# Optimization experiments

Hardware: AMD Instinct MI355X
Metric: run time of the kernel (lower is better)

## Reference

```python
import jax, jax.numpy as jnp
import numpy as np

# Dimensions: B=batch, T=timesteps, D=input_dim, U=units, R=recurrent_size, NE=#edge types
B, T, D, U, R, NE = 1024, 128, 256, 256, 4, 40


def setup_inputs() -> dict:
    key = jax.random.key(0)
    ks = jax.random.split(key, 11)
    s = 1.0 / np.sqrt(U)  # RandomUniform(-1/sqrt(units), 1/sqrt(units)) as in __init__
    inputs = jax.random.normal(ks[0], (B, T, D), jnp.float32)
    input_lengths = jax.random.randint(ks[1], (B,), 1, T + 1)
    # dependencies[b, t, k] indexes a PAST timestep (< t) whose hidden state feeds step t;
    # values >= t are treated as '$' (no dependency -> zero state), matching the string-'$' logic.
    dependencies = jax.random.randint(ks[2], (B, T, R - 1), 0, T)
    edge_types = jax.random.randint(ks[3], (B, T, R), 0, NE)
    mask = jax.random.randint(ks[4], (B, T), 0, 2).astype(bool)
    cell_mask = jax.random.randint(ks[5], (B, T, R), 0, 2).astype(bool)
    Wx = jax.random.uniform(ks[6], (D, 3 * U), jnp.float32, -s, s)   # input kernel (r,z,h)
    Uh = jax.random.uniform(ks[7], (U, 3 * U), jnp.float32, -s, s)   # recurrent kernel (r,z,h)
    Ve = jax.random.uniform(ks[8], (U, 3 * U), jnp.float32, -s, s)   # edge-embedding kernel (r,z,h)
    b = jax.random.uniform(ks[9], (3 * U,), jnp.float32, -s, s)
    edge_emb = jax.random.normal(ks[10], (NE, U), jnp.float32) * 0.02  # shared_emb table
    return dict(inputs=inputs, input_lengths=input_lengths, dependencies=dependencies,
                edge_types=edge_types, mask=mask, cell_mask=cell_mask,
                Wx=Wx, Uh=Uh, Ve=Ve, b=b, edge_emb=edge_emb)


def _graph_gru_forward(inputs, dependencies, edge_types, mask, cell_mask, Wx, Uh, Ve, b, edge_emb):
    Bn, Tn, Dn = inputs.shape
    Un = Uh.shape[0]
    # time-major, as the wrapper does with swap_batch_timestep
    xg_t = jnp.einsum('btd,dg->tbg', inputs, Wx) + b   # precompute input projections [T,B,3U]
    dep_t = jnp.swapaxes(dependencies, 0, 1)           # [T,B,R-1]
    et_t = jnp.swapaxes(edge_types, 0, 1)              # [T,B,R]
    m_t = jnp.swapaxes(mask, 0, 1)                     # [T,B]
    cm_t = jnp.swapaxes(cell_mask, 0, 1)               # [T,B,R]
    bidx = jnp.arange(Bn)

    def step(carry, xs):
        h_prev, H = carry                  # h_prev: [B,U]; H: running history of states [T,B,U]
        t, xg, dep, et, m, cm = xs
        # gather dependency states from history; dep >= t means '$' -> zero state
        valid = dep < t                                        # [B,R-1]
        dep_states = H[jnp.clip(dep, 0, Tn - 1), bidx[:, None]]  # [B,R-1,U]
        dep_states = jnp.where(valid[..., None], dep_states, 0.0)
        hs = jnp.concatenate([h_prev[:, None, :], dep_states], axis=1)  # states tuple -> [B,R,U]
        cmf = cm.astype(hs.dtype)[..., None]                   # per-slot cell mask [B,R,1]
        hs_m = hs * cmf
        e_m = edge_emb[et] * cmf                               # [B,R,U]
        # aggregate messages from the R masked (state, edge-embedding) slots into the 3 gates
        msg = jnp.einsum('bru,ug->bg', hs_m, Uh) + jnp.einsum('bru,ug->bg', e_m, Ve)  # [B,3U]
        xr, xz, xh = jnp.split(xg, 3, axis=-1)
        mr, mz, mh = jnp.split(msg, 3, axis=-1)
        r = jax.nn.sigmoid(xr + mr)
        z = jax.nn.sigmoid(xz + mz)
        hcand = jnp.tanh(xh + r * mh)
        denom = jnp.maximum(cmf.sum(axis=1), 1.0)              # [B,1]
        h_bar = hs_m.sum(axis=1) / denom                       # mean of active predecessor states
        h_new = z * h_bar + (1.0 - z) * hcand
        # masked update: where(mask_t, new_state, previous return state)
        h_out = jnp.where(m[:, None], h_new, h_prev)
        H = H.at[t].set(h_out)
        return (h_out, H), None

    h0 = jnp.zeros((Bn, Un), inputs.dtype)
    H0 = jnp.zeros((Tn, Bn, Un), inputs.dtype)
    (h_last, _), _ = jax.lax.scan(
        step, (h0, H0), (jnp.arange(Tn), xg_t, dep_t, et_t, m_t, cm_t))
    # zero_output_for_mask on the last output (return_sequences=False)
    return jnp.where(m_t[-1][:, None], h_last, 0.0)


def reference(inputs, input_lengths, dependencies, edge_types, mask, cell_mask,
              Wx, Uh, Ve, b, edge_emb):
    # input_lengths only matters when go_backwards=True (default False) -> unused.
    del input_lengths
    return _graph_gru_forward(inputs, dependencies, edge_types, mask, cell_mask,
                              Wx, Uh, Ve, b, edge_emb)
```

## Files before the change

kernel.cpp:

```cpp
#include <hip/hip_runtime.h>
#include <hip/hip_bf16.h>
#include <stdint.h>

typedef _Float16 f16;
typedef _Float16 f16x8 __attribute__((ext_vector_type(8)));
typedef _Float16 f16x4 __attribute__((ext_vector_type(4)));
typedef float    f32x4 __attribute__((ext_vector_type(4)));

#define B_N 1024
#define T_N 128
#define U_N 256
#define G3  768
#define NC  1024
#define KC  512
#define M_N (B_N * T_N)
#define S16P 264

__device__ __forceinline__ void glds16(const void* g, void* l) {
  __builtin_amdgcn_global_load_lds((const __attribute__((address_space(1))) unsigned int*)g,
                                   (__attribute__((address_space(3))) unsigned int*)l, 16, 0, 0);
}
__device__ __forceinline__ void glds4(const void* g, void* l) {
  __builtin_amdgcn_global_load_lds((const __attribute__((address_space(1))) unsigned int*)g,
                                   (__attribute__((address_space(3))) unsigned int*)l, 4, 0, 0);
}

__global__ void k_prep(const float* __restrict__ Wx, const float* __restrict__ Uh,
                       const float* __restrict__ Ve, const float* __restrict__ bsrc,
                       f16* __restrict__ B2, float* __restrict__ bias, f16* __restrict__ UhF)
{
  int idx = blockIdx.x * 256 + threadIdx.x;
  if (idx < NC * KC) {
    int e = idx & 7, slot = (idx >> 3) & 3, r = (idx >> 5) & 127;
    int kt = (idx >> 12) & 15, nt8 = idx >> 16;
    int swz = ((r >> 2) ^ r) & 3;
    int np = nt8 * 128 + r;
    int k  = kt * 32 + ((slot ^ swz) & 3) * 8 + e;
    int u = np >> 2, part = np & 3;
    float v;
    if (part == 0)      v = (k < 256) ? Wx[k * G3 + u]         : Ve[(k - 256) * G3 + u];
    else if (part == 1) v = (k < 256) ? Wx[k * G3 + 256 + u]   : Ve[(k - 256) * G3 + 256 + u];
    else if (part == 2) v = (k < 256) ? Wx[k * G3 + 512 + u]   : 0.f;
    else                v = (k < 256) ? 0.f                    : Ve[(k - 256) * G3 + 512 + u];
    B2[idx] = (f16)v;
    return;
  }
  int i2 = idx - NC * KC;
  if (i2 < U_N * G3) {
    int j = i2 & 7, lane = (i2 >> 3) & 63, fn = i2 >> 9;
    int nt = fn % 6, kkw = fn / 6;
    int kk = kkw & 7, w = kkw >> 3;
    int k = kk * 32 + (lane >> 4) * 8 + j;
    int npp = w * 96 + nt * 16 + (lane & 15);
    int q = npp >> 4;
    int u = (q / 3) * 16 + (npp & 15), gate = q % 3;
    UhF[i2] = (f16)Uh[k * G3 + gate * 256 + u];
    return;
  }
  int i3 = i2 - U_N * G3;
  if (i3 < NC) {
    int u = i3 >> 2, part = i3 & 3;
    bias[i3] = (part < 3) ? bsrc[part * 256 + u] : 0.f;
  }
}

__global__ __launch_bounds__(256) void k_build_a2(const float* __restrict__ inp, const int* __restrict__ et,
                           const int* __restrict__ cmk, const float* __restrict__ emb,
                           f16* __restrict__ A2)
{
  int idx = blockIdx.x * 256 + threadIdx.x;
  int slot = idx & 3, t = (idx >> 2) & 127, kt = (idx >> 9) & 15, b = idx >> 13;
  int swz = ((t >> 2) ^ t) & 3;
  int k0 = kt * 32 + ((slot ^ swz) & 3) * 8;
  int m = b * 128 + t;
  f16x8 v;
  if (k0 < 256) {
    const float* s = inp + (size_t)m * 256 + k0;
    #pragma unroll
    for (int j = 0; j < 8; ++j) v[j] = (f16)s[j];
  } else {
    int c = k0 - 256;
    const int* e  = et  + (size_t)m * 4;
    const int* cm = cmk + (size_t)m * 4;
    float a[8] = {0,0,0,0,0,0,0,0};
    #pragma unroll
    for (int r = 0; r < 4; ++r)
      if (cm[r]) {
        const float* es = emb + e[r] * U_N + c;
        #pragma unroll
        for (int j = 0; j < 8; ++j) a[j] += es[j];
      }
    #pragma unroll
    for (int j = 0; j < 8; ++j) v[j] = (f16)a[j];
  }
  *(f16x8*)(A2 + (size_t)idx * 8) = v;
}

__global__ __launch_bounds__(256) void k_gemm2(const f16* __restrict__ A2,
                                               const f16* __restrict__ B2,
                                               const float* __restrict__ bias,
                                               f16* __restrict__ C)
{
  __shared__ __align__(16) f16 sbuf[3][2][4096];
  const int tid  = threadIdx.x;
  const int lane = tid & 63, wv = tid >> 6;
  const int wm = wv >> 1, wn = wv & 1;
  const int l15 = lane & 15, lhi = lane >> 4;
  const int wg = (blockIdx.x & 7) * 1024 + (blockIdx.x >> 3);
  const int mt = wg >> 3, nt = wg & 7;
  const int m0 = mt * 128, n0 = nt * 128;

  const f16* gabase = A2 + (size_t)mt * 16 * 4096 + wv * 1024 + lane * 8;
  const f16* gbbase = B2 + (size_t)nt * 16 * 4096 + wv * 1024 + lane * 8;

  #define STAGE(kt_, buf_) do {                                             \
    int kk_ = (kt_);                                                        \
    glds16(gabase + (size_t)kk_ * 4096,       &sbuf[buf_][0][wv * 1024]);   \
    glds16(gabase + (size_t)kk_ * 4096 + 512, &sbuf[buf_][0][wv * 1024 + 512]); \
    glds16(gbbase + (size_t)kk_ * 4096,       &sbuf[buf_][1][wv * 1024]);   \
    glds16(gbbase + (size_t)kk_ * 4096 + 512, &sbuf[buf_][1][wv * 1024 + 512]); \
  } while (0)

  f32x4 acc[4][4] = {};

  STAGE(0, 0);
  STAGE(1, 1);
  __builtin_amdgcn_sched_barrier(0);

  int aoff[4], boff[4];
  #pragma unroll
  for (int i = 0; i < 4; ++i) {
    int ar = wm * 64 + i * 16 + l15;
    aoff[i] = ar * 32 + ((lhi ^ ((ar >> 2) ^ ar)) & 3) * 8;
    int br = wn * 64 + i * 16 + l15;
    boff[i] = br * 32 + ((lhi ^ ((br >> 2) ^ br)) & 3) * 8;
  }

  for (int t = 0; t < 16; ++t) {
    const int buf  = t % 3;
    const int bufp = (t + 2) % 3;
    STAGE((t + 2 < 16) ? (t + 2) : 15, bufp);
    __builtin_amdgcn_sched_barrier(0);
    asm volatile("s_waitcnt vmcnt(8)" ::: "memory");
    __builtin_amdgcn_sched_barrier(0);
    __builtin_amdgcn_s_barrier();
    __builtin_amdgcn_sched_barrier(0);

    const f16* sA = &sbuf[buf][0][0];
    const f16* sB = &sbuf[buf][1][0];
    f16x8 af[4], bf[4];
    #pragma unroll
    for (int i = 0; i < 4; ++i) {
      af[i] = *(const f16x8*)(sA + aoff[i]);
      bf[i] = *(const f16x8*)(sB + boff[i]);
    }
    #pragma unroll
    for (int i = 0; i < 4; ++i)
      #pragma unroll
      for (int j = 0; j < 4; ++j)
        acc[i][j] = __builtin_amdgcn_mfma_f32_16x16x32_f16(af[i], bf[j], acc[i][j], 0, 0, 0);

    asm volatile("s_waitcnt lgkmcnt(0)" ::: "memory");
    __builtin_amdgcn_s_barrier();
    __builtin_amdgcn_sched_barrier(0);
  }

  float bv[4];
  #pragma unroll
  for (int j = 0; j < 4; ++j) bv[j] = bias[n0 + wn * 64 + j * 16 + l15];
  asm volatile("s_waitcnt vmcnt(0)" ::: "memory");
  __builtin_amdgcn_sched_barrier(0);
  __builtin_amdgcn_s_barrier();

  f16* ep = &sbuf[0][0][0];
  #pragma unroll
  for (int i = 0; i < 4; ++i)
    #pragma unroll
    for (int j = 0; j < 4; ++j)
      #pragma unroll
      for (int r = 0; r < 4; ++r)
        ep[(wm * 64 + i * 16 + lhi * 4 + r) * 132 + wn * 64 + j * 16 + l15] =
            (f16)(acc[i][j][r] + bv[j]);
  __syncthreads();

  #pragma unroll
  for (int it = 0; it < 8; ++it) {
    int row = it * 16 + (tid >> 4), chunk = tid & 15;
    *(f16x8*)(C + (size_t)(m0 + row) * 1024 + n0 + chunk * 8) =
        *(const f16x8*)(ep + row * 132 + chunk * 8);
  }
  #undef STAGE
}

__global__ __launch_bounds__(512, 2) void k_scan4(
    const f16* __restrict__ pre,
    const f16* __restrict__ UhF,
    const int* __restrict__ dep,
    const int* __restrict__ cmk,
    const int* __restrict__ msk,
    f16* __restrict__ H16,
    float* __restrict__ out)
{
  __shared__ __align__(16) f16 s16[16 * S16P];
  __shared__ __align__(16) f16 hring[2][1024];
  __shared__ __align__(16) f16 dbuf[2][3072];
  __shared__ __align__(16) f16 spre[3][4096];
  __shared__ __align__(16) int sidxl[4][64];
  __shared__ __align__(16) int dpad[64];

  const int tid  = threadIdx.x;
  const int lane = tid & 63, w = tid >> 6;
  const int l15  = lane & 15, lhi = lane >> 4;
  const int b0   = blockIdx.x * 4;

  f16x8 uh[48];
  {
    const f16* ub = UhF + ((size_t)w * 48 * 64 + lane) * 8;
    #pragma unroll
    for (int i = 0; i < 48; ++i) uh[i] = *(const f16x8*)(ub + i * 512);
  }

  ((int*)hring)[tid]       = 0;
  ((int*)hring)[tid + 512] = 0;

  if (tid < 96) {
    int tt = tid >> 5, ll2 = tid & 31, rr = ll2 >> 3, f = ll2 & 7;
    size_t b = b0 + rr;
    int v;
    if (f < 4)      v = cmk[(b * T_N + tt) * 4 + f];
    else if (f < 7) v = dep[(b * T_N + tt) * 3 + (f - 4)];
    else            v = msk[b * T_N + tt];
    sidxl[tt][rr * 8 + f] = v;
  }
  __syncthreads();

  const f16* spre_src = pre + ((size_t)(b0 + (w >> 1)) * T_N) * 1024 + (w & 1) * 512 + lane * 8;
  const int  ll = lane & 31;
  const int  srr = ll >> 3, sf = ll & 7;
  const size_t sb = b0 + srr;
  const int* sidx_base;
  int sidx_stride;
  if (sf < 4)      { sidx_base = cmk + sb * T_N * 4 + sf;       sidx_stride = 4; }
  else if (sf < 7) { sidx_base = dep + sb * T_N * 3 + (sf - 4); sidx_stride = 3; }
  else             { sidx_base = msk + sb * T_N;                sidx_stride = 1; }
  const int dq  = 2 * w + (lane >> 5);
  const int drr = dq / 3, drm = dq - drr * 3;
  const f16* dsrc_base = H16 + (size_t)(b0 + drr) * 256 + (lane & 31) * 8;
  const int strr = ((w - 6) * 64 + lane) >> 5;
  const int stuo = (((w - 6) * 64 + lane) & 31) * 8;

  #pragma unroll
  for (int pr = 0; pr < 2; ++pr)
    glds16(spre_src + (size_t)pr * 1024, &spre[pr][w * 512]);
  #pragma unroll
  for (int i = 0; i < 3; ++i)
    glds4(msk, &dpad[0]);

  for (int t = 0; t < T_N; ++t) {
    asm volatile("s_waitcnt vmcnt(2)" ::: "memory");
    __builtin_amdgcn_sched_barrier(0);

    if (tid < 128) {
      const int rr = tid >> 5, uo = (tid & 31) * 8;
      const int* six = &sidxl[t & 3][rr * 8];
      int cm0 = six[0];
      int cms0 = six[1], cms1 = six[2], cms2 = six[3];
      int dd0 = six[4],  dd1 = six[5],  dd2 = six[6];
      f16x8 hprev = *(const f16x8*)&hring[(t + 1) & 1][rr * 256 + uo];
      f16x8 hold  = *(const f16x8*)&hring[t & 1][rr * 256 + uo];
      f32x4 a0 = {0.f,0.f,0.f,0.f}, a1 = {0.f,0.f,0.f,0.f};
      if (cm0) {
        #pragma unroll
        for (int j = 0; j < 4; ++j) { a0[j] += (float)hprev[j]; a1[j] += (float)hprev[j + 4]; }
      }
      int cma[3] = {cms0, cms1, cms2};
      int dda[3] = {dd0, dd1, dd2};
      #pragma unroll
      for (int r = 0; r < 3; ++r) {
        f16x8 dv = *(const f16x8*)&dbuf[t & 1][(rr * 3 + r) * 256 + uo];
        int d = dda[r];
        f16x8 src = (d == t - 1) ? hprev : ((d == t - 2) ? hold : dv);
        if (cma[r] && (d < t)) {
          #pragma unroll
          for (int j = 0; j < 4; ++j) { a0[j] += (float)src[j]; a1[j] += (float)src[j + 4]; }
        }
      }
      f16x8 s8;
      #pragma unroll
      for (int j = 0; j < 4; ++j) { s8[j] = (f16)a0[j]; s8[j + 4] = (f16)a1[j]; }
      *(f16x8*)&s16[(rr * 4) * S16P + uo] = s8;
    }
    asm volatile("s_waitcnt lgkmcnt(0)" ::: "memory");
    __builtin_amdgcn_s_barrier();
    __builtin_amdgcn_sched_barrier(0);

    if (w < 6) {
      int d = sidxl[(t + 1) & 3][drr * 8 + 4 + drm];
      glds16(dsrc_base + (size_t)d * (B_N * 256), &dbuf[(t + 1) & 1][w * 512]);
    } else {
      f16x8 hv = *(const f16x8*)&hring[(t + 1) & 1][strr * 256 + stuo];
      int tt = (t == 0) ? T_N : (t - 1);
      *(f16x8*)(H16 + ((size_t)tt * B_N + b0 + strr) * 256 + stuo) = hv;
    }
    __builtin_amdgcn_sched_barrier(0);
    {
      int tt2 = (t + 2 < T_N) ? (t + 2) : (T_N - 1);
      glds16(spre_src + (size_t)tt2 * 1024, &spre[(t + 2) % 3][w * 512]);
    }
    __builtin_amdgcn_sched_barrier(0);
    {
      int t3 = (t + 3 < T_N) ? (t + 3) : (T_N - 1);
      glds4(sidx_base + (size_t)t3 * sidx_stride, &sidxl[(t + 3) & 3][0]);
    }
    __builtin_amdgcn_sched_barrier(0);

    f32x4 acc[6];
    #pragma unroll
    for (int i = 0; i < 6; ++i) acc[i] = (f32x4){0.f, 0.f, 0.f, 0.f};
    #pragma unroll
    for (int kk = 0; kk < 8; ++kk) {
      f16x8 a = *(const f16x8*)(s16 + l15 * S16P + kk * 32 + lhi * 8);
      #pragma unroll
      for (int nt = 0; nt < 6; ++nt)
        acc[nt] = __builtin_amdgcn_mfma_f32_16x16x32_f16(a, uh[kk * 6 + nt], acc[nt], 0, 0, 0);
    }

    asm volatile("s_waitcnt vmcnt(7)" ::: "memory");
    __builtin_amdgcn_sched_barrier(0);
    {
      const int* six = &sidxl[t & 3][lhi * 8];
      int c0 = six[0], c1 = six[1], c2 = six[2], c3 = six[3];
      int mfl = six[7];
      float cnt  = (float)(c0 + c1 + c2 + c3);
      float rcnt = __builtin_amdgcn_rcpf(fmaxf(cnt, 1.f));
      #pragma unroll
      for (int ub2 = 0; ub2 < 2; ++ub2) {
        int u = w * 32 + ub2 * 16 + l15;
        f16x4 p = *(const f16x4*)&spre[t % 3][lhi * 1024 + u * 4];
        float mr = acc[ub2 * 3 + 0][0];
        float mz = acc[ub2 * 3 + 1][0];
        float mh = acc[ub2 * 3 + 2][0];
        float tr = (float)p.x + mr;
        float tz = (float)p.y + mz;
        float hx = (float)p.z;
        float he = (float)p.w;
        float rg = __builtin_amdgcn_rcpf(1.f + __expf(-tr));
        float zg = __builtin_amdgcn_rcpf(1.f + __expf(-tz));
        float aa = hx + rg * (mh + he);
        float hc = 2.f * __builtin_amdgcn_rcpf(1.f + __expf(-2.f * aa)) - 1.f;
        float sv = (float)s16[(lhi * 4) * S16P + u];
        float hb = sv * rcnt;
        float hn = zg * hb + (1.f - zg) * hc;
        float hp_ = (float)hring[(t + 1) & 1][lhi * 256 + u];
        float ho = mfl ? hn : hp_;
        hring[t & 1][lhi * 256 + u] = (f16)ho;
      }
    }
    asm volatile("s_waitcnt lgkmcnt(0)" ::: "memory");
    __builtin_amdgcn_s_barrier();
    __builtin_amdgcn_sched_barrier(0);
  }

  if (tid < 128) {
    const int rr = tid >> 5, uo = (tid & 31) * 8;
    int m = sidxl[(T_N - 1) & 3][rr * 8 + 7];
    f16x8 h8 = *(const f16x8*)&hring[(T_N - 1) & 1][rr * 256 + uo];
    f32x4 o0, o1;
    #pragma unroll
    for (int j = 0; j < 4; ++j) {
      o0[j] = m ? (float)h8[j]     : 0.f;
      o1[j] = m ? (float)h8[j + 4] : 0.f;
    }
    *(f32x4*)(out + (size_t)(b0 + rr) * 256 + uo)     = o0;
    *(f32x4*)(out + (size_t)(b0 + rr) * 256 + uo + 4) = o1;
  }
}

extern "C" void kernel_launch(void* const* d_in, const int* in_sizes, int n_in,
                              void* d_out, int out_size, void* d_ws, size_t ws_size,
                              hipStream_t stream)
{
  const float* inputs = (const float*)d_in[0];
  const int*   deps   = (const int*)d_in[2];
  const int*   et     = (const int*)d_in[3];
  const int*   msk    = (const int*)d_in[4];
  const int*   cmk    = (const int*)d_in[5];
  const float* Wx     = (const float*)d_in[6];
  const float* Uh     = (const float*)d_in[7];
  const float* Ve     = (const float*)d_in[8];
  const float* bb     = (const float*)d_in[9];
  const float* emb    = (const float*)d_in[10];
  float* out = (float*)d_out;

  char* ws = (char*)d_ws;
  f16*   A2    = (f16*)ws;
  f16*   H16   = (f16*)ws;
  f16*   pre   = (f16*)(ws + 134217728);
  f16*   B2    = (f16*)(ws + 402653184);
  float* bias  = (float*)(ws + 403701760);
  f16*   UhF   = (f16*)(ws + 403705856);

  int prep_n = NC * KC + U_N * G3 + NC;
  k_prep<<<dim3((prep_n + 255) / 256), dim3(256), 0, stream>>>(Wx, Uh, Ve, bb, B2, bias, UhF);
  k_build_a2<<<dim3(M_N * 64 / 256), dim3(256), 0, stream>>>(inputs, et, cmk, emb, A2);
  k_gemm2<<<dim3((M_N / 128) * (NC / 128)), dim3(256), 0, stream>>>(A2, B2, bias, pre);
  k_scan4<<<dim3(B_N / 4), dim3(512), 0, stream>>>(pre, UhF, deps, cmk, msk, H16, out);
}
```

Measured before the change: 507.3 us.

## Restructure scan kernel to four waves holding doubled recurrent weights in registers

```diff
diff --git a/kernel.cpp b/kernel.cpp
--- a/kernel.cpp
+++ b/kernel.cpp
@@ -19,10 +19,6 @@
 __device__ __forceinline__ void glds16(const void* g, void* l) {
   __builtin_amdgcn_global_load_lds((const __attribute__((address_space(1))) unsigned int*)g,
                                    (__attribute__((address_space(3))) unsigned int*)l, 16, 0, 0);
-}
-__device__ __forceinline__ void glds4(const void* g, void* l) {
-  __builtin_amdgcn_global_load_lds((const __attribute__((address_space(1))) unsigned int*)g,
-                                   (__attribute__((address_space(3))) unsigned int*)l, 4, 0, 0);
 }
 
 __global__ void k_prep(const float* __restrict__ Wx, const float* __restrict__ Uh,
@@ -48,10 +44,10 @@
   int i2 = idx - NC * KC;
   if (i2 < U_N * G3) {
     int j = i2 & 7, lane = (i2 >> 3) & 63, fn = i2 >> 9;
-    int nt = fn % 6, kkw = fn / 6;
+    int nt = fn % 12, kkw = fn / 12;
     int kk = kkw & 7, w = kkw >> 3;
     int k = kk * 32 + (lane >> 4) * 8 + j;
-    int npp = w * 96 + nt * 16 + (lane & 15);
+    int npp = w * 192 + nt * 16 + (lane & 15);
     int q = npp >> 4;
     int u = (q / 3) * 16 + (npp & 15), gate = q % 3;
     UhF[i2] = (f16)Uh[k * G3 + gate * 256 + u];
@@ -154,11 +150,13 @@
       af[i] = *(const f16x8*)(sA + aoff[i]);
       bf[i] = *(const f16x8*)(sB + boff[i]);
     }
+    __builtin_amdgcn_s_setprio(1);
     #pragma unroll
     for (int i = 0; i < 4; ++i)
       #pragma unroll
       for (int j = 0; j < 4; ++j)
         acc[i][j] = __builtin_amdgcn_mfma_f32_16x16x32_f16(af[i], bf[j], acc[i][j], 0, 0, 0);
+    __builtin_amdgcn_s_setprio(0);
 
     asm volatile("s_waitcnt lgkmcnt(0)" ::: "memory");
     __builtin_amdgcn_s_barrier();
@@ -192,7 +190,7 @@
   #undef STAGE
 }
 
-__global__ __launch_bounds__(512, 2) void k_scan4(
+__global__ __launch_bounds__(256, 1) void k_scan7(
     const f16* __restrict__ pre,
     const f16* __restrict__ UhF,
     const int* __restrict__ dep,
@@ -205,56 +203,50 @@
   __shared__ __align__(16) f16 hring[2][1024];
   __shared__ __align__(16) f16 dbuf[2][3072];
   __shared__ __align__(16) f16 spre[3][4096];
-  __shared__ __align__(16) int sidxl[4][64];
-  __shared__ __align__(16) int dpad[64];
+  __shared__ int sidx_all[4][T_N][8];
 
   const int tid  = threadIdx.x;
   const int lane = tid & 63, w = tid >> 6;
   const int l15  = lane & 15, lhi = lane >> 4;
   const int b0   = blockIdx.x * 4;
 
-  f16x8 uh[48];
+  f16x8 uh[96];
   {
-    const f16* ub = UhF + ((size_t)w * 48 * 64 + lane) * 8;
-    #pragma unroll
-    for (int i = 0; i < 48; ++i) uh[i] = *(const f16x8*)(ub + i * 512);
-  }
-
-  ((int*)hring)[tid]       = 0;
-  ((int*)hring)[tid + 512] = 0;
-
-  if (tid < 96) {
-    int tt = tid >> 5, ll2 = tid & 31, rr = ll2 >> 3, f = ll2 & 7;
+    const f16* ub = UhF + (size_t)w * 49152 + lane * 8;
+    #pragma unroll
+    for (int i = 0; i < 96; ++i) uh[i] = *(const f16x8*)(ub + i * 512);
+  }
+
+  for (int i = tid; i < 1024; i += 256) ((int*)hring)[i] = 0;
+  for (int i = tid; i < 2112; i += 256) ((int*)s16)[i] = 0;
+
+  for (int i = tid; i < 4 * T_N * 8; i += 256) {
+    int rr = i >> 10, rem = i & 1023, tt = rem >> 3, f = rem & 7;
     size_t b = b0 + rr;
     int v;
     if (f < 4)      v = cmk[(b * T_N + tt) * 4 + f];
     else if (f < 7) v = dep[(b * T_N + tt) * 3 + (f - 4)];
     else            v = msk[b * T_N + tt];
-    sidxl[tt][rr * 8 + f] = v;
+    sidx_all[rr][tt][f] = v;
   }
   __syncthreads();
-
-  const f16* spre_src = pre + ((size_t)(b0 + (w >> 1)) * T_N) * 1024 + (w & 1) * 512 + lane * 8;
-  const int  ll = lane & 31;
-  const int  srr = ll >> 3, sf = ll & 7;
-  const size_t sb = b0 + srr;
-  const int* sidx_base;
-  int sidx_stride;
-  if (sf < 4)      { sidx_base = cmk + sb * T_N * 4 + sf;       sidx_stride = 4; }
-  else if (sf < 7) { sidx_base = dep + sb * T_N * 3 + (sf - 4); sidx_stride = 3; }
-  else             { sidx_base = msk + sb * T_N;                sidx_stride = 1; }
-  const int dq  = 2 * w + (lane >> 5);
-  const int drr = dq / 3, drm = dq - drr * 3;
-  const f16* dsrc_base = H16 + (size_t)(b0 + drr) * 256 + (lane & 31) * 8;
-  const int strr = ((w - 6) * 64 + lane) >> 5;
-  const int stuo = (((w - 6) * 64 + lane) & 31) * 8;
-
-  #pragma unroll
-  for (int pr = 0; pr < 2; ++pr)
-    glds16(spre_src + (size_t)pr * 1024, &spre[pr][w * 512]);
-  #pragma unroll
-  for (int i = 0; i < 3; ++i)
-    glds4(msk, &dpad[0]);
+  __builtin_amdgcn_sched_barrier(0);
+
+  const f16* spre_src = pre + ((size_t)(b0 + w) * T_N) * 1024 + lane * 8;
+  const int  sprd = w * 1024;
+  const int q0 = 4 * w + (lane >> 5), q1 = q0 + 2;
+  const int r0 = q0 / 3, dm0 = q0 - r0 * 3;
+  const int r1 = q1 / 3, dm1 = q1 - r1 * 3;
+  const f16* dsrc0 = H16 + (size_t)(b0 + (r0 & 3)) * 256 + (lane & 31) * 8;
+  const f16* dsrc1 = H16 + (size_t)(b0 + (r1 & 3)) * 256 + (lane & 31) * 8;
+  const int srow0 = (lane >> 5), srow1 = 2 + (lane >> 5);
+  const int soff  = (lane & 31) * 8;
+
+  glds16(spre_src,        &spre[0][sprd]);
+  glds16(spre_src + 512,  &spre[0][sprd + 512]);
+  glds16(spre_src + 1024, &spre[1][sprd]);
+  glds16(spre_src + 1536, &spre[1][sprd + 512]);
+  __builtin_amdgcn_sched_barrier(0);
 
   for (int t = 0; t < T_N; ++t) {
     asm volatile("s_waitcnt vmcnt(2)" ::: "memory");
@@ -262,10 +254,10 @@
 
     if (tid < 128) {
       const int rr = tid >> 5, uo = (tid & 31) * 8;
-      const int* six = &sidxl[t & 3][rr * 8];
+      const int* six = &sidx_all[rr][t][0];
       int cm0 = six[0];
-      int cms0 = six[1], cms1 = six[2], cms2 = six[3];
-      int dd0 = six[4],  dd1 = six[5],  dd2 = six[6];
+      int cma[3] = {six[1], six[2], six[3]};
+      int dda[3] = {six[4], six[5], six[6]};
       f16x8 hprev = *(const f16x8*)&hring[(t + 1) & 1][rr * 256 + uo];
       f16x8 hold  = *(const f16x8*)&hring[t & 1][rr * 256 + uo];
       f32x4 a0 = {0.f,0.f,0.f,0.f}, a1 = {0.f,0.f,0.f,0.f};
@@ -273,8 +265,6 @@
         #pragma unroll
         for (int j = 0; j < 4; ++j) { a0[j] += (float)hprev[j]; a1[j] += (float)hprev[j + 4]; }
       }
-      int cma[3] = {cms0, cms1, cms2};
-      int dda[3] = {dd0, dd1, dd2};
       #pragma unroll
       for (int r = 0; r < 3; ++r) {
         f16x8 dv = *(const f16x8*)&dbuf[t & 1][(rr * 3 + r) * 256 + uo];
@@ -294,52 +284,53 @@
     __builtin_amdgcn_s_barrier();
     __builtin_amdgcn_sched_barrier(0);
 
-    if (w < 6) {
-      int d = sidxl[(t + 1) & 3][drr * 8 + 4 + drm];
-      glds16(dsrc_base + (size_t)d * (B_N * 256), &dbuf[(t + 1) & 1][w * 512]);
+    if (w < 3) {
+      int tn = (t + 1 < T_N) ? (t + 1) : (T_N - 1);
+      int d0v = sidx_all[r0][tn][4 + dm0];
+      glds16(dsrc0 + (size_t)d0v * (B_N * 256), &dbuf[(t + 1) & 1][(4 * w) * 256]);
+      int d1v = sidx_all[r1][tn][4 + dm1];
+      glds16(dsrc1 + (size_t)d1v * (B_N * 256), &dbuf[(t + 1) & 1][(4 * w + 2) * 256]);
     } else {
-      f16x8 hv = *(const f16x8*)&hring[(t + 1) & 1][strr * 256 + stuo];
       int tt = (t == 0) ? T_N : (t - 1);
-      *(f16x8*)(H16 + ((size_t)tt * B_N + b0 + strr) * 256 + stuo) = hv;
+      f16x8 hv0 = *(const f16x8*)&hring[(t + 1) & 1][srow0 * 256 + soff];
+      *(f16x8*)(H16 + ((size_t)tt * B_N + b0 + srow0) * 256 + soff) = hv0;
+      f16x8 hv1 = *(const f16x8*)&hring[(t + 1) & 1][srow1 * 256 + soff];
+      *(f16x8*)(H16 + ((size_t)tt * B_N + b0 + srow1) * 256 + soff) = hv1;
     }
     __builtin_amdgcn_sched_barrier(0);
     {
-      int tt2 = (t + 2 < T_N) ? (t + 2) : (T_N - 1);
-      glds16(spre_src + (size_t)tt2 * 1024, &spre[(t + 2) % 3][w * 512]);
-    }
-    __builtin_amdgcn_sched_barrier(0);
-    {
-      int t3 = (t + 3 < T_N) ? (t + 3) : (T_N - 1);
-      glds4(sidx_base + (size_t)t3 * sidx_stride, &sidxl[(t + 3) & 3][0]);
-    }
-    __builtin_amdgcn_sched_barrier(0);
-
-    f32x4 acc[6];
-    #pragma unroll
-    for (int i = 0; i < 6; ++i) acc[i] = (f32x4){0.f, 0.f, 0.f, 0.f};
+      int t2 = (t + 2 < T_N) ? (t + 2) : (T_N - 1);
+      glds16(spre_src + (size_t)t2 * 1024,       &spre[(t + 2) % 3][sprd]);
+      glds16(spre_src + (size_t)t2 * 1024 + 512, &spre[(t + 2) % 3][sprd + 512]);
+    }
+    __builtin_amdgcn_sched_barrier(0);
+
+    f32x4 acc[12];
+    #pragma unroll
+    for (int i = 0; i < 12; ++i) acc[i] = (f32x4){0.f, 0.f, 0.f, 0.f};
+    __builtin_amdgcn_s_setprio(1);
     #pragma unroll
     for (int kk = 0; kk < 8; ++kk) {
       f16x8 a = *(const f16x8*)(s16 + l15 * S16P + kk * 32 + lhi * 8);
       #pragma unroll
-      for (int nt = 0; nt < 6; ++nt)
-        acc[nt] = __builtin_amdgcn_mfma_f32_16x16x32_f16(a, uh[kk * 6 + nt], acc[nt], 0, 0, 0);
-    }
-
-    asm volatile("s_waitcnt vmcnt(7)" ::: "memory");
-    __builtin_amdgcn_sched_barrier(0);
+      for (int nt = 0; nt < 12; ++nt)
+        acc[nt] = __builtin_amdgcn_mfma_f32_16x16x32_f16(a, uh[kk * 12 + nt], acc[nt], 0, 0, 0);
+    }
+    __builtin_amdgcn_s_setprio(0);
+
     {
-      const int* six = &sidxl[t & 3][lhi * 8];
+      const int* six = &sidx_all[lhi][t][0];
       int c0 = six[0], c1 = six[1], c2 = six[2], c3 = six[3];
       int mfl = six[7];
       float cnt  = (float)(c0 + c1 + c2 + c3);
       float rcnt = __builtin_amdgcn_rcpf(fmaxf(cnt, 1.f));
       #pragma unroll
-      for (int ub2 = 0; ub2 < 2; ++ub2) {
-        int u = w * 32 + ub2 * 16 + l15;
+      for (int ub = 0; ub < 4; ++ub) {
+        int u = w * 64 + ub * 16 + l15;
         f16x4 p = *(const f16x4*)&spre[t % 3][lhi * 1024 + u * 4];
-        float mr = acc[ub2 * 3 + 0][0];
-        float mz = acc[ub2 * 3 + 1][0];
-        float mh = acc[ub2 * 3 + 2][0];
+        float mr = acc[3 * ub + 0][0];
+        float mz = acc[3 * ub + 1][0];
+        float mh = acc[3 * ub + 2][0];
         float tr = (float)p.x + mr;
         float tz = (float)p.y + mz;
         float hx = (float)p.z;
@@ -363,7 +354,7 @@
 
   if (tid < 128) {
     const int rr = tid >> 5, uo = (tid & 31) * 8;
-    int m = sidxl[(T_N - 1) & 3][rr * 8 + 7];
+    int m = sidx_all[rr][T_N - 1][7];
     f16x8 h8 = *(const f16x8*)&hring[(T_N - 1) & 1][rr * 256 + uo];
     f32x4 o0, o1;
     #pragma unroll
@@ -404,5 +395,5 @@
   k_prep<<<dim3((prep_n + 255) / 256), dim3(256), 0, stream>>>(Wx, Uh, Ve, bb, B2, bias, UhF);
   k_build_a2<<<dim3(M_N * 64 / 256), dim3(256), 0, stream>>>(inputs, et, cmk, emb, A2);
   k_gemm2<<<dim3((M_N / 128) * (NC / 128)), dim3(256), 0, stream>>>(A2, B2, bias, pre);
-  k_scan4<<<dim3(B_N / 4), dim3(512), 0, stream>>>(pre, UhF, deps, cmk, msk, H16, out);
-}
+  k_scan7<<<dim3(B_N / 4), dim3(256), 0, stream>>>(pre, UhF, deps, cmk, msk, H16, out);
+}
```

After: 610.3 us. +20.3%, slower.
